# Kernel tuning notes

Hardware: AMD Instinct MI355X
Metric: run time of the kernel (lower is better)

## Reference

```python
import math
import jax, jax.numpy as jnp
import numpy as np

HIDDEN = 1024
N_HEADS = 16
HEAD_DIM = HIDDEN // N_HEADS
SEQ = 2048
BATCH = 2
MAX_SEQ = 2048
N_LAYERS = 4
ALPHA = 0.3
TOPK_FACTOR = 2
GAMMA = 0.5
M_FREQ = math.ceil(MAX_SEQ / 2) + 1  # rfft length


def _sample_indices(layer_idx):
    # FrequencyRampSampler.get_sample_indices (layer_idx is a static python int)
    l = layer_idx + 1
    M, L = M_FREQ, N_LAYERS
    if ALPHA > 1.0 / L:
        p = int(M * (1 - ALPHA) * (1 - (l - 1) / (L - 1))) if L > 1 else 0
        q = int(p + ALPHA * M)
    else:
        p = int(M * (1 - l / L))
        q = int(p + M / L)
    p = max(0, min(p, M - 1))
    q = max(p + 1, min(q, M))
    return p, q


def setup_inputs() -> dict:
    key = jax.random.key(0)
    ks = jax.random.split(key, 10)
    hidden_states = jax.random.normal(ks[0], (BATCH, SEQ, HIDDEN), jnp.float32)
    # causal additive mask [B,1,N,N]
    causal = jnp.tril(jnp.ones((SEQ, SEQ), jnp.float32))
    attention_mask = jnp.where(causal > 0, 0.0, -1e9).astype(jnp.float32)
    attention_mask = jnp.broadcast_to(attention_mask[None, None], (BATCH, 1, SEQ, SEQ))
    s = 0.02
    Wq = jax.random.normal(ks[1], (HIDDEN, HIDDEN), jnp.float32) * s
    Wk = jax.random.normal(ks[2], (HIDDEN, HIDDEN), jnp.float32) * s
    Wv = jax.random.normal(ks[3], (HIDDEN, HIDDEN), jnp.float32) * s
    Wo = jax.random.normal(ks[4], (HIDDEN, HIDDEN), jnp.float32) * s
    bq = jnp.zeros((HIDDEN,), jnp.float32)
    bk = jnp.zeros((HIDDEN,), jnp.float32)
    bv = jnp.zeros((HIDDEN,), jnp.float32)
    bo = jnp.zeros((HIDDEN,), jnp.float32)
    return dict(hidden_states=hidden_states, attention_mask=attention_mask,
                Wq=Wq, bq=bq, Wk=Wk, bk=bk, Wv=Wv, bv=bv, Wo=Wo, bo=bo,
                layer_idx=1)


def _forward(hidden_states, attention_mask, Wq, bq, Wk, bk, Wv, bv, Wo, bo, layer_idx):
    B, N, D = hidden_states.shape
    p, q = _sample_indices(layer_idx)
    Q = hidden_states @ Wq.T + bq
    K = hidden_states @ Wk.T + bk
    V = hidden_states @ Wv.T + bv

    # ---- time-domain branch: FFT -> band-select -> IFFT -> SDPA ----
    def band_filter(X):
        Xf = jnp.fft.rfft(X, axis=1)  # [B, M, D] complex64
        Xp = jnp.zeros_like(Xf).at[:, p:q, :].set(Xf[:, p:q, :])
        return jnp.fft.irfft(Xp, n=N, axis=1)

    Qt = band_filter(Q).reshape(B, N, N_HEADS, HEAD_DIM).transpose(0, 2, 1, 3)
    Kt = band_filter(K).reshape(B, N, N_HEADS, HEAD_DIM).transpose(0, 2, 1, 3)
    Vt = band_filter(V).reshape(B, N, N_HEADS, HEAD_DIM).transpose(0, 2, 1, 3)
    scores = jnp.einsum('bhnd,bhmd->bhnm', Qt, Kt) / math.sqrt(HEAD_DIM)
    scores = scores + attention_mask
    probs = jax.nn.softmax(scores, axis=-1)
    time_out = jnp.einsum('bhnm,bhmd->bhnd', probs, Vt)
    time_out = time_out.transpose(0, 2, 1, 3).reshape(B, N, D)

    # ---- frequency-domain branch: autocorrelation + top-k delay aggregation ----
    Qf = jnp.fft.rfft(Q, axis=1)
    Kf = jnp.fft.rfft(K, axis=1)
    corr = jnp.zeros_like(Qf).at[:, p:q, :].set(Qf[:, p:q, :] * jnp.conj(Kf[:, p:q, :]))
    R = jnp.fft.irfft(corr, n=N, axis=1)          # [B, N, D]
    R_mean = R.mean(axis=-1)                       # [B, N]
    k = min(max(1, int(TOPK_FACTOR * math.log(N + 1))), N)
    top_R, top_idx = jax.lax.top_k(R_mean, k)      # [B, k]
    attn_w = jax.nn.softmax(top_R, axis=-1)        # [B, k]
    # rolled index: (n - tau) mod N, for each of the k delays
    idx = (jnp.arange(N)[None, None, :] - top_idx[:, :, None]) % N   # [B, k, N]
    gathered = jnp.take_along_axis(V[:, None, :, :], idx[..., None], axis=2)  # [B, k, N, D]
    freq_out = jnp.einsum('bk,bknd->bnd', attn_w, gathered)

    out = GAMMA * time_out + (1.0 - GAMMA) * freq_out
    return out @ Wo.T + bo


def reference(hidden_states, attention_mask, Wq, bq, Wk, bk, Wv, bv, Wo, bo, layer_idx):
    return _forward(hidden_states, attention_mask, Wq, bq, Wk, bk, Wv, bv, Wo, bo, layer_idx)
```

## Files before the change

kernel.cpp:

```cpp
#include <hip/hip_runtime.h>
#include <hip/hip_bf16.h>

#define BATCHN 2
#define SEQ    2048
#define HID    1024
#define NHEADS 16
#define HD     64
#define P_LO   478
#define NF     307
#define NF2    614
#define NFP    640
#define KTOP   15
#define DPI    3.14159265358979323846

typedef __bf16 bf16_t;
typedef bf16_t v8bf __attribute__((ext_vector_type(8)));
typedef bf16_t v4bf __attribute__((ext_vector_type(4)));
typedef float  v4f  __attribute__((ext_vector_type(4)));

#define MFMA(a,b,c) __builtin_amdgcn_mfma_f32_16x16x32_bf16(a,b,c,0,0,0)

#define GLDS(gp, lp) __builtin_amdgcn_global_load_lds( \
    (const __attribute__((address_space(1))) void*)(gp), \
    (__attribute__((address_space(3))) void*)(lp), 16, 0, 0)

__launch_bounds__(256)
__global__ void detect_kernel(const unsigned short* __restrict__ x0,
                              const unsigned short* __restrict__ x1,
                              int* __restrict__ flag) {
    int t = threadIdx.x, bad = 0;
    for (int i = t; i < 8192; i += 256) {
        unsigned e0 = (x0[i] >> 7) & 0xFF; if (e0 >= 0x90) bad++;
        unsigned e1 = (x1[i] >> 7) & 0xFF; if (e1 >= 0x90) bad++;
    }
    __shared__ int s[256];
    s[t] = bad; __syncthreads();
    for (int st = 128; st; st >>= 1) { if (t < st) s[t] += s[t + st]; __syncthreads(); }
    if (t == 0) *flag = (s[0] > 64) ? 1 : 0;
}

__launch_bounds__(256)
__global__ void tab_kernel(bf16_t* __restrict__ Ahi, bf16_t* __restrict__ Alo,
                           bf16_t* __restrict__ Gt) {
    __shared__ float T[64 * 65];
    int t = threadIdx.x;
    int m0 = blockIdx.x * 64, r0 = blockIdx.y * 64;
    int m = t >> 2, rb = (t & 3) * 16;
    {
        v8bf g0, g1;
        #pragma unroll
        for (int i = 0; i < 16; i++) {
            int r = r0 + rb + i;
            float v = 0.f;
            if (r < NF2) {
                int f  = P_LO + (r < NF ? r : r - NF);
                int ph = (f * (m0 + m)) & (SEQ - 1);
                float ang = (float)(2.0 * DPI / SEQ) * (float)ph;
                float sn, cs;
                sincosf(ang, &sn, &cs);
                v = (r < NF) ? cs : sn;
            }
            T[(rb + i) * 65 + m] = v;
            bf16_t gv = (bf16_t)(v * (float)(2.0 / SEQ));
            if (i < 8) g0[i] = gv; else g1[i - 8] = gv;
        }
        *(v8bf*)&Gt[(size_t)(m0 + m) * NFP + r0 + rb]     = g0;
        *(v8bf*)&Gt[(size_t)(m0 + m) * NFP + r0 + rb + 8] = g1;
    }
    __syncthreads();
    int r = t >> 2, mb = (t & 3) * 16;
    v8bf h0, h1, l0, l1;
    #pragma unroll
    for (int i = 0; i < 16; i++) {
        float v = T[r * 65 + mb + i];
        bf16_t hh = (bf16_t)v;
        bf16_t ll = (bf16_t)(v - (float)hh);
        if (i < 8) { h0[i] = hh; l0[i] = ll; } else { h1[i - 8] = hh; l1[i - 8] = ll; }
    }
    size_t ro = (size_t)(r0 + r) * SEQ + m0 + mb;
    *(v8bf*)&Ahi[ro]     = h0;  *(v8bf*)&Ahi[ro + 8] = h1;
    *(v8bf*)&Alo[ro]     = l0;  *(v8bf*)&Alo[ro + 8] = l1;
}

__launch_bounds__(256)
__global__ void norm_x_kernel(const int* __restrict__ flag, const void* __restrict__ Xv,
                              bf16_t* __restrict__ Xh, bf16_t* __restrict__ XTh,
                              bf16_t* __restrict__ XTl) {
    int fl = *flag;
    __shared__ float T[64 * 65];
    int t = threadIdx.x;
    int R0 = blockIdx.y * 64, C0 = blockIdx.x * 64;
    int r = t >> 2;
    #pragma unroll
    for (int it = 0; it < 2; it++) {
        int c = (t & 3) * 8 + it * 32;
        float x[8];
        if (fl) {
            const float* p = (const float*)Xv + (size_t)(R0 + r) * HID + C0 + c;
            #pragma unroll
            for (int e = 0; e < 8; e++) x[e] = p[e];
        } else {
            const bf16_t* p = (const bf16_t*)Xv + (size_t)(R0 + r) * HID + C0 + c;
            #pragma unroll
            for (int e = 0; e < 8; e++) x[e] = (float)p[e];
        }
        v8bf h;
        #pragma unroll
        for (int e = 0; e < 8; e++) { h[e] = (bf16_t)x[e]; T[(r) * 65 + c + e] = x[e]; }
        *(v8bf*)&Xh[(size_t)(R0 + r) * HID + C0 + c] = h;
    }
    __syncthreads();
    int b  = blockIdx.y >> 5;
    int Rl = R0 - b * SEQ;
    int d  = t >> 2;
    #pragma unroll
    for (int it = 0; it < 2; it++) {
        int n = (t & 3) * 8 + it * 32;
        v8bf h, l;
        #pragma unroll
        for (int e = 0; e < 8; e++) {
            float x = T[(n + e) * 65 + d];
            bf16_t hh = (bf16_t)x;
            h[e] = hh; l[e] = (bf16_t)(x - (float)hh);
        }
        size_t off = ((size_t)b * HID + C0 + d) * SEQ + Rl + n;
        *(v8bf*)&XTh[off] = h;
        *(v8bf*)&XTl[off] = l;
    }
}

__launch_bounds__(256)
__global__ void gemm128_nt(const int* __restrict__ flag, const bf16_t* __restrict__ A,
                           const void* __restrict__ Braw, const void* __restrict__ biasraw,
                           void* __restrict__ Out, int outmode) {
    int fl = *flag;
    __shared__ __align__(16) bf16_t As[128 * 32];
    __shared__ __align__(16) bf16_t Bs[128 * 32];
    int t = threadIdx.x, wave = t >> 6, lane = t & 63;
    int lrow = lane & 15, quad = lane >> 4;
    int m0 = blockIdx.y * 128, n0 = blockIdx.x * 128;
    int wm = (wave >> 1) * 64, wn = (wave & 1) * 64;
    int grow = lane >> 2, gcol = (lane & 3) * 8;
    v4f acc[4][4] = {};
    for (int k0 = 0; k0 < HID; k0 += 32) {
        __syncthreads();
        GLDS(&A[(size_t)(m0 + wave * 32 + grow) * HID + k0 + gcol],      &As[(wave * 32) * 32]);
        GLDS(&A[(size_t)(m0 + wave * 32 + 16 + grow) * HID + k0 + gcol], &As[(wave * 32 + 16) * 32]);
        if (!fl) {
            const bf16_t* B = (const bf16_t*)Braw;
            GLDS(&B[(size_t)(n0 + wave * 32 + grow) * HID + k0 + gcol],      &Bs[(wave * 32) * 32]);
            GLDS(&B[(size_t)(n0 + wave * 32 + 16 + grow) * HID + k0 + gcol], &Bs[(wave * 32 + 16) * 32]);
        } else {
            const float* B = (const float*)Braw;
            #pragma unroll
            for (int i2 = 0; i2 < 2; i2++) {
                int row = (t >> 2) + 64 * i2, col = (t & 3) * 8;
                const float* p = &B[(size_t)(n0 + row) * HID + k0 + col];
                v8bf h;
                #pragma unroll
                for (int e = 0; e < 8; e++) h[e] = (bf16_t)p[e];
                *(v8bf*)&Bs[row * 32 + col] = h;
            }
        }
        __syncthreads();
        v8bf a[4], b[4];
        #pragma unroll
        for (int i = 0; i < 4; i++) a[i] = *(v8bf*)&As[(wm + i * 16 + lrow) * 32 + quad * 8];
        #pragma unroll
        for (int j = 0; j < 4; j++) b[j] = *(v8bf*)&Bs[(wn + j * 16 + lrow) * 32 + quad * 8];
        #pragma unroll
        for (int i = 0; i < 4; i++)
        #pragma unroll
        for (int j = 0; j < 4; j++) acc[i][j] = MFMA(a[i], b[j], acc[i][j]);
    }
    #pragma unroll
    for (int i = 0; i < 4; i++)
    #pragma unroll
    for (int j = 0; j < 4; j++) {
        int col = n0 + wn + 16 * j + lrow;
        float bvv = fl ? ((const float*)biasraw)[col] : (float)((const bf16_t*)biasraw)[col];
        #pragma unroll
        for (int rg = 0; rg < 4; rg++) {
            int row = m0 + wm + 16 * i + quad * 4 + rg;
            float v = acc[i][j][rg] + bvv;
            size_t off = (size_t)row * HID + col;
            if (outmode == 1 && fl) ((float*)Out)[off] = v;
            else ((bf16_t*)Out)[off] = (bf16_t)v;
        }
    }
}

__launch_bounds__(256)
__global__ void band_fwd(const bf16_t* __restrict__ Ahi, const bf16_t* __restrict__ Alo,
                         const bf16_t* __restrict__ XTh, const bf16_t* __restrict__ XTl,
                         bf16_t* __restrict__ Xfh, bf16_t* __restrict__ Xfl) {
    __shared__ __align__(16) bf16_t Ah[64 * 32], Al[64 * 32], Bh[64 * 32], Bl[64 * 32];
    int t = threadIdx.x, wave = t >> 6, lane = t & 63;
    int lrow = lane & 15, quad = lane >> 4;
    int m0 = blockIdx.y * 64, n0 = blockIdx.x * 64, b = blockIdx.z;
    int wm = (wave >> 1) * 32, wn = (wave & 1) * 32;
    int srow = t >> 2, scol = (t & 3) * 8;
    const bf16_t* bth = XTh + (size_t)b * HID * SEQ;
    const bf16_t* btl = XTl + (size_t)b * HID * SEQ;
    v4f acc[2][2] = {};
    for (int k0 = 0; k0 < SEQ; k0 += 32) {
        __syncthreads();
        GLDS(&Ahi[(size_t)(m0 + srow) * SEQ + k0 + scol], &Ah[srow * 32 + scol]);
        GLDS(&Alo[(size_t)(m0 + srow) * SEQ + k0 + scol], &Al[srow * 32 + scol]);
        GLDS(&bth[(size_t)(n0 + srow) * SEQ + k0 + scol], &Bh[srow * 32 + scol]);
        GLDS(&btl[(size_t)(n0 + srow) * SEQ + k0 + scol], &Bl[srow * 32 + scol]);
        __syncthreads();
        v8bf ah0 = *(v8bf*)&Ah[(wm + lrow) * 32 + quad * 8];
        v8bf ah1 = *(v8bf*)&Ah[(wm + 16 + lrow) * 32 + quad * 8];
        v8bf al0 = *(v8bf*)&Al[(wm + lrow) * 32 + quad * 8];
        v8bf al1 = *(v8bf*)&Al[(wm + 16 + lrow) * 32 + quad * 8];
        v8bf bh0 = *(v8bf*)&Bh[(wn + lrow) * 32 + quad * 8];
        v8bf bh1 = *(v8bf*)&Bh[(wn + 16 + lrow) * 32 + quad * 8];
        v8bf bl0 = *(v8bf*)&Bl[(wn + lrow) * 32 + quad * 8];
        v8bf bl1 = *(v8bf*)&Bl[(wn + 16 + lrow) * 32 + quad * 8];
        acc[0][0] = MFMA(ah0, bh0, acc[0][0]); acc[0][0] = MFMA(ah0, bl0, acc[0][0]); acc[0][0] = MFMA(al0, bh0, acc[0][0]);
        acc[0][1] = MFMA(ah0, bh1, acc[0][1]); acc[0][1] = MFMA(ah0, bl1, acc[0][1]); acc[0][1] = MFMA(al0, bh1, acc[0][1]);
        acc[1][0] = MFMA(ah1, bh0, acc[1][0]); acc[1][0] = MFMA(ah1, bl0, acc[1][0]); acc[1][0] = MFMA(al1, bh0, acc[1][0]);
        acc[1][1] = MFMA(ah1, bh1, acc[1][1]); acc[1][1] = MFMA(ah1, bl1, acc[1][1]); acc[1][1] = MFMA(al1, bh1, acc[1][1]);
    }
    bf16_t* oh = Xfh + (size_t)b * NFP * HID;
    bf16_t* ol = Xfl + (size_t)b * NFP * HID;
    #pragma unroll
    for (int i = 0; i < 2; i++)
    #pragma unroll
    for (int j = 0; j < 2; j++) {
        int col = n0 + wn + 16 * j + lrow;
        #pragma unroll
        for (int rg = 0; rg < 4; rg++) {
            int row = m0 + wm + 16 * i + quad * 4 + rg;
            float v = acc[i][j][rg];
            bf16_t h = (bf16_t)v;
            oh[(size_t)row * HID + col] = h;
            ol[(size_t)row * HID + col] = (bf16_t)(v - (float)h);
        }
    }
}

__launch_bounds__(256)
__global__ void proj_f(const int* __restrict__ flag, const bf16_t* __restrict__ Xfh,
                       const bf16_t* __restrict__ Xfl,
                       const void* __restrict__ Wq_, const void* __restrict__ Wk_,
                       const void* __restrict__ Wv_,
                       bf16_t* __restrict__ Qfh, bf16_t* __restrict__ Qfl,
                       bf16_t* __restrict__ Kfh, bf16_t* __restrict__ Kfl,
                       bf16_t* __restrict__ QfT, bf16_t* __restrict__ KfT,
                       bf16_t* __restrict__ VfT) {
    int fl = *flag;
    int bz = blockIdx.z, b = bz & 1, sel = bz >> 1;
    const void* Wraw = sel == 0 ? Wq_ : sel == 1 ? Wk_ : Wv_;
    bf16_t* Ch = sel == 0 ? Qfh : Kfh;
    bf16_t* Cl = sel == 0 ? Qfl : Kfl;
    bf16_t* CT = sel == 0 ? QfT : sel == 1 ? KfT : VfT;
    bool qk = sel < 2;
    __shared__ __align__(16) bf16_t Ah[64 * 32], Al[64 * 32], Bh[64 * 32], Bl[64 * 32];
    int t = threadIdx.x, wave = t >> 6, lane = t & 63;
    int lrow = lane & 15, quad = lane >> 4;
    int m0 = blockIdx.y * 64, n0 = blockIdx.x * 64;
    int wm = (wave >> 1) * 32, wn = (wave & 1) * 32;
    int srow = t >> 2, scol = (t & 3) * 8;
    const size_t zo = (size_t)b * NFP * HID;
    v4f acc[2][2] = {};
    for (int k0 = 0; k0 < HID; k0 += 32) {
        __syncthreads();
        GLDS(&Xfh[zo + (size_t)(m0 + srow) * HID + k0 + scol], &Ah[srow * 32 + scol]);
        GLDS(&Xfl[zo + (size_t)(m0 + srow) * HID + k0 + scol], &Al[srow * 32 + scol]);
        {
            float xb[8];
            if (fl) {
                const float* p = (const float*)Wraw + (size_t)(n0 + srow) * HID + k0 + scol;
                #pragma unroll
                for (int e = 0; e < 8; e++) xb[e] = p[e];
            } else {
                const bf16_t* p = (const bf16_t*)Wraw + (size_t)(n0 + srow) * HID + k0 + scol;
                #pragma unroll
                for (int e = 0; e < 8; e++) xb[e] = (float)p[e];
            }
            v8bf h, l;
            #pragma unroll
            for (int e = 0; e < 8; e++) {
                bf16_t hh = (bf16_t)xb[e];
                h[e] = hh; l[e] = (bf16_t)(xb[e] - (float)hh);
            }
            *(v8bf*)&Bh[srow * 32 + scol] = h;
            *(v8bf*)&Bl[srow * 32 + scol] = l;
        }
        __syncthreads();
        v8bf ah0 = *(v8bf*)&Ah[(wm + lrow) * 32 + quad * 8];
        v8bf ah1 = *(v8bf*)&Ah[(wm + 16 + lrow) * 32 + quad * 8];
        v8bf al0 = *(v8bf*)&Al[(wm + lrow) * 32 + quad * 8];
        v8bf al1 = *(v8bf*)&Al[(wm + 16 + lrow) * 32 + quad * 8];
        v8bf bh0 = *(v8bf*)&Bh[(wn + lrow) * 32 + quad * 8];
        v8bf bh1 = *(v8bf*)&Bh[(wn + 16 + lrow) * 32 + quad * 8];
        acc[0][0] = MFMA(ah0, bh0, acc[0][0]); acc[0][0] = MFMA(al0, bh0, acc[0][0]);
        acc[0][1] = MFMA(ah0, bh1, acc[0][1]); acc[0][1] = MFMA(al0, bh1, acc[0][1]);
        acc[1][0] = MFMA(ah1, bh0, acc[1][0]); acc[1][0] = MFMA(al1, bh0, acc[1][0]);
        acc[1][1] = MFMA(ah1, bh1, acc[1][1]); acc[1][1] = MFMA(al1, bh1, acc[1][1]);
        if (qk) {
            v8bf bl0 = *(v8bf*)&Bl[(wn + lrow) * 32 + quad * 8];
            v8bf bl1 = *(v8bf*)&Bl[(wn + 16 + lrow) * 32 + quad * 8];
            acc[0][0] = MFMA(ah0, bl0, acc[0][0]);
            acc[0][1] = MFMA(ah0, bl1, acc[0][1]);
            acc[1][0] = MFMA(ah1, bl0, acc[1][0]);
            acc[1][1] = MFMA(ah1, bl1, acc[1][1]);
        }
    }
    #pragma unroll
    for (int i = 0; i < 2; i++)
    #pragma unroll
    for (int j = 0; j < 2; j++) {
        int col = n0 + wn + 16 * j + lrow;
        v4bf pk;
        #pragma unroll
        for (int rg = 0; rg < 4; rg++) {
            int row = m0 + wm + 16 * i + quad * 4 + rg;
            float v = acc[i][j][rg];
            bf16_t h = (bf16_t)v;
            pk[rg] = h;
            if (qk) {
                Ch[zo + (size_t)row * HID + col] = h;
                Cl[zo + (size_t)row * HID + col] = (bf16_t)(v - (float)h);
            }
        }
        *(v4bf*)&CT[zo + (size_t)col * NFP + m0 + wm + 16 * i + quad * 4] = pk;
    }
}

__launch_bounds__(256)
__global__ void inv128_f(const bf16_t* __restrict__ Gt, const bf16_t* __restrict__ QfT,
                         const bf16_t* __restrict__ KfT, const bf16_t* __restrict__ VfT,
                         bf16_t* __restrict__ Qt, bf16_t* __restrict__ Kt,
                         bf16_t* __restrict__ VTd) {
    int bz = blockIdx.z, b = bz & 1, sel = bz >> 1;
    const bf16_t* BT = (sel == 0 ? QfT : sel == 1 ? KfT : VfT) + (size_t)b * HID * NFP;
    bf16_t* Out = sel == 0 ? Qt : sel == 1 ? Kt : VTd;
    bool trans = (sel == 2);
    __shared__ __align__(16) bf16_t As[128 * 32];
    __shared__ __align__(16) bf16_t Bs[128 * 32];
    int t = threadIdx.x, wave = t >> 6, lane = t & 63;
    int lrow = lane & 15, quad = lane >> 4;
    int m0 = blockIdx.y * 128, n0 = blockIdx.x * 128;
    int wm = (wave >> 1) * 64, wn = (wave & 1) * 64;
    int grow = lane >> 2, gcol = (lane & 3) * 8;
    v4f acc[4][4] = {};
    for (int k0 = 0; k0 < NFP; k0 += 32) {
        __syncthreads();
        GLDS(&Gt[(size_t)(m0 + wave * 32 + grow) * NFP + k0 + gcol],      &As[(wave * 32) * 32]);
        GLDS(&Gt[(size_t)(m0 + wave * 32 + 16 + grow) * NFP + k0 + gcol], &As[(wave * 32 + 16) * 32]);
        GLDS(&BT[(size_t)(n0 + wave * 32 + grow) * NFP + k0 + gcol],      &Bs[(wave * 32) * 32]);
        GLDS(&BT[(size_t)(n0 + wave * 32 + 16 + grow) * NFP + k0 + gcol], &Bs[(wave * 32 + 16) * 32]);
        __syncthreads();
        v8bf a[4], bfr[4];
        #pragma unroll
        for (int i = 0; i < 4; i++) a[i]   = *(v8bf*)&As[(wm + i * 16 + lrow) * 32 + quad * 8];
        #pragma unroll
        for (int j = 0; j < 4; j++) bfr[j] = *(v8bf*)&Bs[(wn + j * 16 + lrow) * 32 + quad * 8];
        #pragma unroll
        for (int i = 0; i < 4; i++)
        #pragma unroll
        for (int j = 0; j < 4; j++) acc[i][j] = MFMA(a[i], bfr[j], acc[i][j]);
    }
    #pragma unroll
    for (int i = 0; i < 4; i++)
    #pragma unroll
    for (int j = 0; j < 4; j++) {
        int col = n0 + wn + 16 * j + lrow;
        if (trans) {
            v4bf pk;
            #pragma unroll
            for (int rg = 0; rg < 4; rg++) pk[rg] = (bf16_t)acc[i][j][rg];
            *(v4bf*)&Out[((size_t)b * HID + col) * SEQ + m0 + wm + 16 * i + quad * 4] = pk;
        } else {
            #pragma unroll
            for (int rg = 0; rg < 4; rg++) {
                int row = m0 + wm + 16 * i + quad * 4 + rg;
                Out[(size_t)b * SEQ * HID + (size_t)row * HID + col] = (bf16_t)acc[i][j][rg];
            }
        }
    }
}

__launch_bounds__(256)
__global__ void attn_kernel(const bf16_t* __restrict__ Qt, const bf16_t* __restrict__ Kt,
                            const bf16_t* __restrict__ VT, bf16_t* __restrict__ TO) {
    __shared__ __align__(16) bf16_t Ks[2][64 * 72];
    __shared__ __align__(16) bf16_t Vs[2][64 * 72];
    __shared__ __align__(16) bf16_t Ps[4 * 16 * 72];
    int t = threadIdx.x, wave = t >> 6, lane = t & 63;
    int lrow = lane & 15, quad = lane >> 4;
    int h = blockIdx.y, b = blockIdx.z;
    int q0 = (gridDim.x - 1 - blockIdx.x) * 128;
    const size_t base = (size_t)b * SEQ * HID + (size_t)h * HD;
    const bf16_t* vb_ = VT + ((size_t)b * HID + h * HD) * SEQ;
    bf16_t* Pw = &Ps[wave * 16 * 72];

    v8bf qa[2][2];
    #pragma unroll
    for (int g = 0; g < 2; g++) {
        int qrow = q0 + g * 64 + wave * 16 + lrow;
        qa[g][0] = *(const v8bf*)&Qt[base + (size_t)qrow * HID + quad * 8];
        qa[g][1] = *(const v8bf*)&Qt[base + (size_t)qrow * HID + 32 + quad * 8];
    }
    v4f o[2][4] = {};
    float m_i[2] = {-1e30f, -1e30f}, l_i[2] = {0.f, 0.f};
    int srow = t >> 2, cc0 = (t & 3) * 16;
    int nch = q0 / 64 + 2;
    v8bf kp0 = *(const v8bf*)&Kt[base + (size_t)srow * HID + cc0];
    v8bf kp1 = *(const v8bf*)&Kt[base + (size_t)srow * HID + cc0 + 8];
    v8bf vp0 = *(const v8bf*)&vb_[(size_t)srow * SEQ + cc0];
    v8bf vp1 = *(const v8bf*)&vb_[(size_t)srow * SEQ + cc0 + 8];
    for (int c = 0; c < nch; c++) {
        int kb = c * 64;
        int cur = c & 1;
        *(v8bf*)&Ks[cur][srow * 72 + cc0]     = kp0;
        *(v8bf*)&Ks[cur][srow * 72 + cc0 + 8] = kp1;
        *(v8bf*)&Vs[cur][srow * 72 + cc0]     = vp0;
        *(v8bf*)&Vs[cur][srow * 72 + cc0 + 8] = vp1;
        __syncthreads();
        if (c + 1 < nch) {
            int kb2 = kb + 64;
            kp0 = *(const v8bf*)&Kt[base + (size_t)(kb2 + srow) * HID + cc0];
            kp1 = *(const v8bf*)&Kt[base + (size_t)(kb2 + srow) * HID + cc0 + 8];
            vp0 = *(const v8bf*)&vb_[(size_t)srow * SEQ + kb2 + cc0];
            vp1 = *(const v8bf*)&vb_[(size_t)srow * SEQ + kb2 + cc0 + 8];
        }
        v8bf kA[4][2], vB[4][2];
        #pragma unroll
        for (int ct = 0; ct < 4; ct++) {
            kA[ct][0] = *(v8bf*)&Ks[cur][(ct * 16 + lrow) * 72 + quad * 8];
            kA[ct][1] = *(v8bf*)&Ks[cur][(ct * 16 + lrow) * 72 + 32 + quad * 8];
            vB[ct][0] = *(v8bf*)&Vs[cur][(ct * 16 + lrow) * 72 + quad * 8];
            vB[ct][1] = *(v8bf*)&Vs[cur][(ct * 16 + lrow) * 72 + 32 + quad * 8];
        }
        #pragma unroll
        for (int g = 0; g < 2; g++) {
            if (kb >= q0 + g * 64 + 64) continue;
            bool masked = (kb == q0 + g * 64);
            v4f s[4];
            #pragma unroll
            for (int ct = 0; ct < 4; ct++) {
                v4f z = {};
                z = MFMA(kA[ct][0], qa[g][0], z);
                s[ct] = MFMA(kA[ct][1], qa[g][1], z);
            }
            float sv[4][4];
            float mx = -1e30f;
            #pragma unroll
            for (int ct = 0; ct < 4; ct++)
            #pragma unroll
            for (int r = 0; r < 4; r++) {
                float x = s[ct][r] * 0.125f;
                if (masked && (ct * 16 + quad * 4 + r > wave * 16 + lrow)) x = -1e30f;
                sv[ct][r] = x;
                mx = fmaxf(mx, x);
            }
            mx = fmaxf(mx, __shfl_xor(mx, 16));
            mx = fmaxf(mx, __shfl_xor(mx, 32));
            float mnew = fmaxf(m_i[g], mx);
            float alpha = __expf(m_i[g] - mnew);
            m_i[g] = mnew;
            float rs = 0.f;
            #pragma unroll
            for (int ct = 0; ct < 4; ct++)
            #pragma unroll
            for (int r = 0; r < 4; r++) { float p = __expf(sv[ct][r] - mnew); sv[ct][r] = p; rs += p; }
            rs += __shfl_xor(rs, 16);
            rs += __shfl_xor(rs, 32);
            l_i[g] = l_i[g] * alpha + rs;
            #pragma unroll
            for (int r = 0; r < 4; r++) {
                float ar = __shfl(alpha, quad * 4 + r);
                #pragma unroll
                for (int dt = 0; dt < 4; dt++) o[g][dt][r] *= ar;
            }
            #pragma unroll
            for (int ct = 0; ct < 4; ct++) {
                v4bf pk;
                #pragma unroll
                for (int r = 0; r < 4; r++) pk[r] = (bf16_t)sv[ct][r];
                *(v4bf*)&Pw[lrow * 72 + ct * 16 + quad * 4] = pk;
            }
            v8bf pa0 = *(v8bf*)&Pw[lrow * 72 + quad * 8];
            v8bf pa1 = *(v8bf*)&Pw[lrow * 72 + 32 + quad * 8];
            #pragma unroll
            for (int dt = 0; dt < 4; dt++) {
                o[g][dt] = MFMA(pa0, vB[dt][0], o[g][dt]);
                o[g][dt] = MFMA(pa1, vB[dt][1], o[g][dt]);
            }
        }
        __syncthreads();
    }
    #pragma unroll
    for (int g = 0; g < 2; g++)
    #pragma unroll
    for (int r = 0; r < 4; r++) {
        float lr = __shfl(l_i[g], quad * 4 + r);
        int qg = q0 + g * 64 + wave * 16 + quad * 4 + r;
        #pragma unroll
        for (int dt = 0; dt < 4; dt++)
            TO[base + (size_t)qg * HID + dt * 16 + lrow] = (bf16_t)(o[g][dt][r] / lr);
    }
}

__launch_bounds__(256)
__global__ void sfreq_kernel(const bf16_t* __restrict__ Qh, const bf16_t* __restrict__ Ql,
                             const bf16_t* __restrict__ Kh, const bf16_t* __restrict__ Kl,
                             float* __restrict__ Sre, float* __restrict__ Sim) {
    int f = blockIdx.x, b = blockIdx.y, t = threadIdx.x;
    const size_t oc = ((size_t)b * NFP + f) * HID;
    const size_t os = ((size_t)b * NFP + NF + f) * HID;
    float re = 0.f, im = 0.f;
    for (int d = t; d < HID; d += 256) {
        float cq = (float)Qh[oc + d] + (float)Ql[oc + d];
        float sq = (float)Qh[os + d] + (float)Ql[os + d];
        float ck = (float)Kh[oc + d] + (float)Kl[oc + d];
        float sk = (float)Kh[os + d] + (float)Kl[os + d];
        re += cq * ck + sq * sk;
        im += cq * sk - sq * ck;
    }
    #pragma unroll
    for (int msk = 1; msk < 64; msk <<= 1) { re += __shfl_xor(re, msk); im += __shfl_xor(im, msk); }
    __shared__ float rbuf[8];
    int wave = t >> 6, lane = t & 63;
    if (lane == 0) { rbuf[wave] = re; rbuf[4 + wave] = im; }
    __syncthreads();
    if (t == 0) {
        Sre[b * NF + f] = rbuf[0] + rbuf[1] + rbuf[2] + rbuf[3];
        Sim[b * NF + f] = rbuf[4] + rbuf[5] + rbuf[6] + rbuf[7];
    }
}

__launch_bounds__(256)
__global__ void rmean_kernel(const float* __restrict__ Sre, const float* __restrict__ Sim,
                             float* __restrict__ Rm) {
    int b = blockIdx.y;
    int nl = threadIdx.x & 63, part = threadIdx.x >> 6;
    int n = blockIdx.x * 64 + nl;
    __shared__ float sr[NF], si[NF];
    __shared__ float red[4][64];
    for (int i = threadIdx.x; i < NF; i += 256) { sr[i] = Sre[b * NF + i]; si[i] = Sim[b * NF + i]; }
    __syncthreads();
    float acc = 0.f;
    for (int r = part; r < NF; r += 4) {
        int ph = ((P_LO + r) * n) & (SEQ - 1);
        float ang = (float)(2.0 * DPI / SEQ) * (float)ph;
        float sn, cs;
        sincosf(ang, &sn, &cs);
        acc += sr[r] * cs - si[r] * sn;
    }
    red[part][nl] = acc;
    __syncthreads();
    if (part == 0) {
        float s = red[0][nl] + red[1][nl] + red[2][nl] + red[3][nl];
        Rm[b * SEQ + n] = s * (float)(2.0 / ((double)SEQ * (double)HID));
    }
}

__launch_bounds__(64)
__global__ void topk_kernel(const float* __restrict__ Rm, int* __restrict__ Ti,
                            float* __restrict__ Tw) {
    int b = blockIdx.x, lane = threadIdx.x;
    float v[32];
    #pragma unroll
    for (int j = 0; j < 32; j++) v[j] = Rm[b * SEQ + j * 64 + lane];
    float selv[KTOP];
    int   seli[KTOP];
    for (int kk = 0; kk < KTOP; kk++) {
        float best = -INFINITY; int bi = lane;
        #pragma unroll
        for (int j = 0; j < 32; j++) {
            float x = v[j];
            if (x > best) { best = x; bi = j * 64 + lane; }
        }
        #pragma unroll
        for (int off = 1; off < 64; off <<= 1) {
            float ov = __shfl_xor(best, off);
            int   oi = __shfl_xor(bi, off);
            if (ov > best || (ov == best && oi < bi)) { best = ov; bi = oi; }
        }
        selv[kk] = best; seli[kk] = bi;
        if (lane == (bi & 63)) v[bi >> 6] = -INFINITY;
    }
    float mx = selv[0];
    #pragma unroll
    for (int i = 1; i < KTOP; i++) mx = fmaxf(mx, selv[i]);
    float s = 0.f, e[KTOP];
    #pragma unroll
    for (int i = 0; i < KTOP; i++) { e[i] = __expf(selv[i] - mx); s += e[i]; }
    if (lane < KTOP) { Tw[b * KTOP + lane] = e[lane] / s; Ti[b * KTOP + lane] = seli[lane]; }
}

__launch_bounds__(256)
__global__ void combine_kernel(const bf16_t* __restrict__ TO, const bf16_t* __restrict__ V,
                               const int* __restrict__ Ti, const float* __restrict__ Tw,
                               bf16_t* __restrict__ Yc) {
    int b = blockIdx.z, n = blockIdx.y;
    int d = blockIdx.x * 256 + threadIdx.x;
    __shared__ int   ti[KTOP];
    __shared__ float tw[KTOP];
    if (threadIdx.x < KTOP) { ti[threadIdx.x] = Ti[b * KTOP + threadIdx.x]; tw[threadIdx.x] = Tw[b * KTOP + threadIdx.x]; }
    __syncthreads();
    float fo = 0.f;
    #pragma unroll
    for (int kk = 0; kk < KTOP; kk++) {
        int nn = (n - ti[kk] + SEQ) & (SEQ - 1);
        fo += tw[kk] * (float)V[((size_t)b * SEQ + nn) * HID + d];
    }
    size_t off = ((size_t)b * SEQ + n) * HID + d;
    Yc[off] = (bf16_t)(0.5f * (float)TO[off] + 0.5f * fo);
}

extern "C" void kernel_launch(void* const* d_in, const int* in_sizes, int n_in,
                              void* d_out, int out_size, void* d_ws, size_t ws_size,
                              hipStream_t stream) {
    (void)in_sizes; (void)n_in; (void)out_size; (void)ws_size;
    const void* X  = d_in[0];
    const void* Wq = d_in[2];
    const void* Wk = d_in[4];
    const void* Wv = d_in[6];
    const void* bv = d_in[7];
    const void* Wo = d_in[8];
    const void* bo = d_in[9];

    const size_t SZ_X   = (size_t)BATCHN * SEQ * HID * 2;
    const size_t SZ_TAB = (size_t)NFP * SEQ * 2;
    const size_t SZ_F   = (size_t)BATCHN * NFP * HID * 2;
    char* w = (char*)d_ws;
    bf16_t* Xh  = (bf16_t*)(w);
    bf16_t* Xfh = (bf16_t*)(w);
    bf16_t* Xfl = (bf16_t*)(w + SZ_F);
    bf16_t* Qt  = (bf16_t*)(w);
    bf16_t* Yc  = (bf16_t*)(w);
    bf16_t* XTh = (bf16_t*)(w + SZ_X);
    bf16_t* Qfh = (bf16_t*)(w + SZ_X);
    bf16_t* Qfl = (bf16_t*)(w + SZ_X + SZ_F);
    bf16_t* Kfh = (bf16_t*)(w + SZ_X + 2 * SZ_F);
    bf16_t* Kt  = (bf16_t*)(w + SZ_X);
    bf16_t* XTl = (bf16_t*)(w + 2 * SZ_X);
    bf16_t* Kfl = (bf16_t*)(w + 2 * SZ_X);
    bf16_t* QfT = (bf16_t*)(w + 2 * SZ_X + SZ_F);
    bf16_t* KfT = (bf16_t*)(w + 2 * SZ_X + 2 * SZ_F);
    bf16_t* TO  = (bf16_t*)(w + 2 * SZ_X);
    bf16_t* Vm  = (bf16_t*)(w + 3 * SZ_X);
    bf16_t* Gt  = (bf16_t*)(w + 4 * SZ_X);
    bf16_t* Ahi = (bf16_t*)(w + 4 * SZ_X + SZ_TAB);
    bf16_t* Alo = (bf16_t*)(w + 4 * SZ_X + 2 * SZ_TAB);
    bf16_t* VfT = (bf16_t*)(w + 4 * SZ_X + SZ_TAB);
    char*  sm  = w + 4 * SZ_X + 3 * SZ_TAB;
    int*   flag = (int*)sm;
    float* Sre  = (float*)(sm + 256);
    float* Sim  = (float*)(sm + 256 + 4096);
    float* Rm   = (float*)(sm + 256 + 8192);
    int*   Ti   = (int*)  (sm + 256 + 8192 + 16384);
    float* Tw   = (float*)(sm + 256 + 8192 + 16384 + 256);
    bf16_t* VT  = (bf16_t*)d_out;

    detect_kernel<<<1, 256, 0, stream>>>((const unsigned short*)X, (const unsigned short*)Wq, flag);
    tab_kernel<<<dim3(SEQ / 64, NFP / 64), 256, 0, stream>>>(Ahi, Alo, Gt);
    norm_x_kernel<<<dim3(16, 64), 256, 0, stream>>>(flag, X, Xh, XTh, XTl);
    gemm128_nt<<<dim3(8, 32), 256, 0, stream>>>(flag, Xh, Wv, bv, Vm, 0);
    band_fwd<<<dim3(16, NFP / 64, BATCHN), 256, 0, stream>>>(Ahi, Alo, XTh, XTl, Xfh, Xfl);
    proj_f<<<dim3(16, NFP / 64, 6), 256, 0, stream>>>(flag, Xfh, Xfl, Wq, Wk, Wv,
                                                      Qfh, Qfl, Kfh, Kfl, QfT, KfT, VfT);
    sfreq_kernel<<<dim3(NF, BATCHN), 256, 0, stream>>>(Qfh, Qfl, Kfh, Kfl, Sre, Sim);
    rmean_kernel<<<dim3(SEQ / 64, BATCHN), 256, 0, stream>>>(Sre, Sim, Rm);
    topk_kernel<<<BATCHN, 64, 0, stream>>>(Rm, Ti, Tw);
    inv128_f<<<dim3(8, 16, 6), 256, 0, stream>>>(Gt, QfT, KfT, VfT, Qt, Kt, VT);
    attn_kernel<<<dim3(SEQ / 128, NHEADS, BATCHN), 256, 0, stream>>>(Qt, Kt, VT, TO);
    combine_kernel<<<dim3(HID / 256, SEQ, BATCHN), 256, 0, stream>>>(TO, Vm, Ti, Tw, Yc);
    gemm128_nt<<<dim3(8, 32), 256, 0, stream>>>(flag, Yc, Wo, bo, d_out, 1);
}
```

Measured before the change: 433.7 us.

## Merge independent stages into block-indexed mega kernels and vectorize combine

Folds detect, table generation, input normalization and the V projection into one launch whose blocks dispatch on block index, with each block re-deriving the input-dtype flag locally. The inverse transform is merged with the rmean reduction, and top-k with attention, in two more such kernels. The V GEMM now reads and converts X directly, dropping the Xh staging copy. The combine kernel handles 8 elements per thread with vector loads, and attention uses exp2f. The goal is fewer launches and better overlap of independent work, at the cost of redundant flag detection in many blocks and mixed block shapes sharing one launch.

```diff
diff --git a/kernel.cpp b/kernel.cpp
--- a/kernel.cpp
+++ b/kernel.cpp
@@ -12,6 +12,7 @@
 #define NFP    640
 #define KTOP   15
 #define DPI    3.14159265358979323846
+#define L2E    1.44269504f
 
 typedef __bf16 bf16_t;
 typedef bf16_t v8bf __attribute__((ext_vector_type(8)));
@@ -24,27 +25,25 @@
     (const __attribute__((address_space(1))) void*)(gp), \
     (__attribute__((address_space(3))) void*)(lp), 16, 0, 0)
 
-__launch_bounds__(256)
-__global__ void detect_kernel(const unsigned short* __restrict__ x0,
-                              const unsigned short* __restrict__ x1,
-                              int* __restrict__ flag) {
+__device__ __forceinline__ int self_detect(const unsigned short* __restrict__ x, char* SM) {
+    int* s = (int*)SM;
     int t = threadIdx.x, bad = 0;
     for (int i = t; i < 8192; i += 256) {
-        unsigned e0 = (x0[i] >> 7) & 0xFF; if (e0 >= 0x90) bad++;
-        unsigned e1 = (x1[i] >> 7) & 0xFF; if (e1 >= 0x90) bad++;
-    }
-    __shared__ int s[256];
+        unsigned e = (x[i] >> 7) & 0xFF;
+        if (e >= 0x90) bad++;
+    }
     s[t] = bad; __syncthreads();
     for (int st = 128; st; st >>= 1) { if (t < st) s[t] += s[t + st]; __syncthreads(); }
-    if (t == 0) *flag = (s[0] > 64) ? 1 : 0;
-}
-
-__launch_bounds__(256)
-__global__ void tab_kernel(bf16_t* __restrict__ Ahi, bf16_t* __restrict__ Alo,
-                           bf16_t* __restrict__ Gt) {
-    __shared__ float T[64 * 65];
+    int r = (s[0] > 32) ? 1 : 0;
+    __syncthreads();
+    return r;
+}
+
+__device__ __forceinline__ void tab_body(int bi, char* SM, bf16_t* Ahi, bf16_t* Alo,
+                                         bf16_t* Gt) {
+    float* T = (float*)SM;
     int t = threadIdx.x;
-    int m0 = blockIdx.x * 64, r0 = blockIdx.y * 64;
+    int m0 = (bi & 31) * 64, r0 = (bi >> 5) * 64;
     int m = t >> 2, rb = (t & 3) * 16;
     {
         v8bf g0, g1;
@@ -82,14 +81,11 @@
     *(v8bf*)&Alo[ro]     = l0;  *(v8bf*)&Alo[ro + 8] = l1;
 }
 
-__launch_bounds__(256)
-__global__ void norm_x_kernel(const int* __restrict__ flag, const void* __restrict__ Xv,
-                              bf16_t* __restrict__ Xh, bf16_t* __restrict__ XTh,
-                              bf16_t* __restrict__ XTl) {
-    int fl = *flag;
-    __shared__ float T[64 * 65];
+__device__ __forceinline__ void norm_body(int bi, int fl, char* SM, const void* Xv,
+                                          bf16_t* XTh, bf16_t* XTl) {
+    float* T = (float*)SM;
     int t = threadIdx.x;
-    int R0 = blockIdx.y * 64, C0 = blockIdx.x * 64;
+    int C0 = (bi & 15) * 64, R0 = (bi >> 4) * 64;
     int r = t >> 2;
     #pragma unroll
     for (int it = 0; it < 2; it++) {
@@ -104,13 +100,11 @@
             #pragma unroll
             for (int e = 0; e < 8; e++) x[e] = (float)p[e];
         }
-        v8bf h;
-        #pragma unroll
-        for (int e = 0; e < 8; e++) { h[e] = (bf16_t)x[e]; T[(r) * 65 + c + e] = x[e]; }
-        *(v8bf*)&Xh[(size_t)(R0 + r) * HID + C0 + c] = h;
+        #pragma unroll
+        for (int e = 0; e < 8; e++) T[r * 65 + c + e] = x[e];
     }
     __syncthreads();
-    int b  = blockIdx.y >> 5;
+    int b  = (R0 >= SEQ) ? 1 : 0;
     int Rl = R0 - b * SEQ;
     int d  = t >> 2;
     #pragma unroll
@@ -129,37 +123,39 @@
     }
 }
 
-__launch_bounds__(256)
-__global__ void gemm128_nt(const int* __restrict__ flag, const bf16_t* __restrict__ A,
-                           const void* __restrict__ Braw, const void* __restrict__ biasraw,
-                           void* __restrict__ Out, int outmode) {
-    int fl = *flag;
-    __shared__ __align__(16) bf16_t As[128 * 32];
-    __shared__ __align__(16) bf16_t Bs[128 * 32];
+__device__ __forceinline__ void gemmv_body(int bi, int fl, char* SM, const void* Xraw,
+                                           const void* Braw, const void* biasraw,
+                                           bf16_t* Out) {
+    bf16_t* As = (bf16_t*)SM;
+    bf16_t* Bs = (bf16_t*)(SM + 8192);
     int t = threadIdx.x, wave = t >> 6, lane = t & 63;
     int lrow = lane & 15, quad = lane >> 4;
-    int m0 = blockIdx.y * 128, n0 = blockIdx.x * 128;
+    int n0 = (bi & 7) * 128, m0 = (bi >> 3) * 128;
     int wm = (wave >> 1) * 64, wn = (wave & 1) * 64;
     int grow = lane >> 2, gcol = (lane & 3) * 8;
     v4f acc[4][4] = {};
     for (int k0 = 0; k0 < HID; k0 += 32) {
         __syncthreads();
-        GLDS(&A[(size_t)(m0 + wave * 32 + grow) * HID + k0 + gcol],      &As[(wave * 32) * 32]);
-        GLDS(&A[(size_t)(m0 + wave * 32 + 16 + grow) * HID + k0 + gcol], &As[(wave * 32 + 16) * 32]);
         if (!fl) {
+            const bf16_t* A = (const bf16_t*)Xraw;
             const bf16_t* B = (const bf16_t*)Braw;
+            GLDS(&A[(size_t)(m0 + wave * 32 + grow) * HID + k0 + gcol],      &As[(wave * 32) * 32]);
+            GLDS(&A[(size_t)(m0 + wave * 32 + 16 + grow) * HID + k0 + gcol], &As[(wave * 32 + 16) * 32]);
             GLDS(&B[(size_t)(n0 + wave * 32 + grow) * HID + k0 + gcol],      &Bs[(wave * 32) * 32]);
             GLDS(&B[(size_t)(n0 + wave * 32 + 16 + grow) * HID + k0 + gcol], &Bs[(wave * 32 + 16) * 32]);
         } else {
+            const float* A = (const float*)Xraw;
             const float* B = (const float*)Braw;
             #pragma unroll
             for (int i2 = 0; i2 < 2; i2++) {
                 int row = (t >> 2) + 64 * i2, col = (t & 3) * 8;
-                const float* p = &B[(size_t)(n0 + row) * HID + k0 + col];
-                v8bf h;
+                const float* pa = &A[(size_t)(m0 + row) * HID + k0 + col];
+                const float* pb = &B[(size_t)(n0 + row) * HID + k0 + col];
+                v8bf ha, hb;
                 #pragma unroll
-                for (int e = 0; e < 8; e++) h[e] = (bf16_t)p[e];
-                *(v8bf*)&Bs[row * 32 + col] = h;
+                for (int e = 0; e < 8; e++) { ha[e] = (bf16_t)pa[e]; hb[e] = (bf16_t)pb[e]; }
+                *(v8bf*)&As[row * 32 + col] = ha;
+                *(v8bf*)&Bs[row * 32 + col] = hb;
             }
         }
         __syncthreads();
@@ -182,11 +178,41 @@
         #pragma unroll
         for (int rg = 0; rg < 4; rg++) {
             int row = m0 + wm + 16 * i + quad * 4 + rg;
-            float v = acc[i][j][rg] + bvv;
-            size_t off = (size_t)row * HID + col;
-            if (outmode == 1 && fl) ((float*)Out)[off] = v;
-            else ((bf16_t*)Out)[off] = (bf16_t)v;
-        }
+            Out[(size_t)row * HID + col] = (bf16_t)(acc[i][j][rg] + bvv);
+        }
+    }
+}
+
+__launch_bounds__(256)
+__global__ void mega1_kernel(const void* __restrict__ X, const void* __restrict__ Wq,
+                             const void* __restrict__ Wv, const void* __restrict__ bv,
+                             bf16_t* __restrict__ Vm,
+                             bf16_t* __restrict__ Ahi, bf16_t* __restrict__ Alo,
+                             bf16_t* __restrict__ Gt,
+                             bf16_t* __restrict__ XTh, bf16_t* __restrict__ XTl,
+                             int* __restrict__ flag) {
+    __shared__ __align__(16) char SM[17408];
+    int bx = blockIdx.x;
+    if (bx < 256) {
+        int fl = self_detect((const unsigned short*)X, SM);
+        gemmv_body(bx, fl, SM, X, Wv, bv, Vm);
+    } else if (bx < 576) {
+        tab_body(bx - 256, SM, Ahi, Alo, Gt);
+    } else if (bx < 1600) {
+        int fl = self_detect((const unsigned short*)X, SM);
+        norm_body(bx - 576, fl, SM, X, XTh, XTl);
+    } else {
+        const unsigned short* x0 = (const unsigned short*)X;
+        const unsigned short* x1 = (const unsigned short*)Wq;
+        int* s = (int*)SM;
+        int t = threadIdx.x, bad = 0;
+        for (int i = t; i < 8192; i += 256) {
+            unsigned e0 = (x0[i] >> 7) & 0xFF; if (e0 >= 0x90) bad++;
+            unsigned e1 = (x1[i] >> 7) & 0xFF; if (e1 >= 0x90) bad++;
+        }
+        s[t] = bad; __syncthreads();
+        for (int st = 128; st; st >>= 1) { if (t < st) s[t] += s[t + st]; __syncthreads(); }
+        if (t == 0) *flag = (s[0] > 64) ? 1 : 0;
     }
 }
 
@@ -331,182 +357,6 @@
 }
 
 __launch_bounds__(256)
-__global__ void inv128_f(const bf16_t* __restrict__ Gt, const bf16_t* __restrict__ QfT,
-                         const bf16_t* __restrict__ KfT, const bf16_t* __restrict__ VfT,
-                         bf16_t* __restrict__ Qt, bf16_t* __restrict__ Kt,
-                         bf16_t* __restrict__ VTd) {
-    int bz = blockIdx.z, b = bz & 1, sel = bz >> 1;
-    const bf16_t* BT = (sel == 0 ? QfT : sel == 1 ? KfT : VfT) + (size_t)b * HID * NFP;
-    bf16_t* Out = sel == 0 ? Qt : sel == 1 ? Kt : VTd;
-    bool trans = (sel == 2);
-    __shared__ __align__(16) bf16_t As[128 * 32];
-    __shared__ __align__(16) bf16_t Bs[128 * 32];
-    int t = threadIdx.x, wave = t >> 6, lane = t & 63;
-    int lrow = lane & 15, quad = lane >> 4;
-    int m0 = blockIdx.y * 128, n0 = blockIdx.x * 128;
-    int wm = (wave >> 1) * 64, wn = (wave & 1) * 64;
-    int grow = lane >> 2, gcol = (lane & 3) * 8;
-    v4f acc[4][4] = {};
-    for (int k0 = 0; k0 < NFP; k0 += 32) {
-        __syncthreads();
-        GLDS(&Gt[(size_t)(m0 + wave * 32 + grow) * NFP + k0 + gcol],      &As[(wave * 32) * 32]);
-        GLDS(&Gt[(size_t)(m0 + wave * 32 + 16 + grow) * NFP + k0 + gcol], &As[(wave * 32 + 16) * 32]);
-        GLDS(&BT[(size_t)(n0 + wave * 32 + grow) * NFP + k0 + gcol],      &Bs[(wave * 32) * 32]);
-        GLDS(&BT[(size_t)(n0 + wave * 32 + 16 + grow) * NFP + k0 + gcol], &Bs[(wave * 32 + 16) * 32]);
-        __syncthreads();
-        v8bf a[4], bfr[4];
-        #pragma unroll
-        for (int i = 0; i < 4; i++) a[i]   = *(v8bf*)&As[(wm + i * 16 + lrow) * 32 + quad * 8];
-        #pragma unroll
-        for (int j = 0; j < 4; j++) bfr[j] = *(v8bf*)&Bs[(wn + j * 16 + lrow) * 32 + quad * 8];
-        #pragma unroll
-        for (int i = 0; i < 4; i++)
-        #pragma unroll
-        for (int j = 0; j < 4; j++) acc[i][j] = MFMA(a[i], bfr[j], acc[i][j]);
-    }
-    #pragma unroll
-    for (int i = 0; i < 4; i++)
-    #pragma unroll
-    for (int j = 0; j < 4; j++) {
-        int col = n0 + wn + 16 * j + lrow;
-        if (trans) {
-            v4bf pk;
-            #pragma unroll
-            for (int rg = 0; rg < 4; rg++) pk[rg] = (bf16_t)acc[i][j][rg];
-            *(v4bf*)&Out[((size_t)b * HID + col) * SEQ + m0 + wm + 16 * i + quad * 4] = pk;
-        } else {
-            #pragma unroll
-            for (int rg = 0; rg < 4; rg++) {
-                int row = m0 + wm + 16 * i + quad * 4 + rg;
-                Out[(size_t)b * SEQ * HID + (size_t)row * HID + col] = (bf16_t)acc[i][j][rg];
-            }
-        }
-    }
-}
-
-__launch_bounds__(256)
-__global__ void attn_kernel(const bf16_t* __restrict__ Qt, const bf16_t* __restrict__ Kt,
-                            const bf16_t* __restrict__ VT, bf16_t* __restrict__ TO) {
-    __shared__ __align__(16) bf16_t Ks[2][64 * 72];
-    __shared__ __align__(16) bf16_t Vs[2][64 * 72];
-    __shared__ __align__(16) bf16_t Ps[4 * 16 * 72];
-    int t = threadIdx.x, wave = t >> 6, lane = t & 63;
-    int lrow = lane & 15, quad = lane >> 4;
-    int h = blockIdx.y, b = blockIdx.z;
-    int q0 = (gridDim.x - 1 - blockIdx.x) * 128;
-    const size_t base = (size_t)b * SEQ * HID + (size_t)h * HD;
-    const bf16_t* vb_ = VT + ((size_t)b * HID + h * HD) * SEQ;
-    bf16_t* Pw = &Ps[wave * 16 * 72];
-
-    v8bf qa[2][2];
-    #pragma unroll
-    for (int g = 0; g < 2; g++) {
-        int qrow = q0 + g * 64 + wave * 16 + lrow;
-        qa[g][0] = *(const v8bf*)&Qt[base + (size_t)qrow * HID + quad * 8];
-        qa[g][1] = *(const v8bf*)&Qt[base + (size_t)qrow * HID + 32 + quad * 8];
-    }
-    v4f o[2][4] = {};
-    float m_i[2] = {-1e30f, -1e30f}, l_i[2] = {0.f, 0.f};
-    int srow = t >> 2, cc0 = (t & 3) * 16;
-    int nch = q0 / 64 + 2;
-    v8bf kp0 = *(const v8bf*)&Kt[base + (size_t)srow * HID + cc0];
-    v8bf kp1 = *(const v8bf*)&Kt[base + (size_t)srow * HID + cc0 + 8];
-    v8bf vp0 = *(const v8bf*)&vb_[(size_t)srow * SEQ + cc0];
-    v8bf vp1 = *(const v8bf*)&vb_[(size_t)srow * SEQ + cc0 + 8];
-    for (int c = 0; c < nch; c++) {
-        int kb = c * 64;
-        int cur = c & 1;
-        *(v8bf*)&Ks[cur][srow * 72 + cc0]     = kp0;
-        *(v8bf*)&Ks[cur][srow * 72 + cc0 + 8] = kp1;
-        *(v8bf*)&Vs[cur][srow * 72 + cc0]     = vp0;
-        *(v8bf*)&Vs[cur][srow * 72 + cc0 + 8] = vp1;
-        __syncthreads();
-        if (c + 1 < nch) {
-            int kb2 = kb + 64;
-            kp0 = *(const v8bf*)&Kt[base + (size_t)(kb2 + srow) * HID + cc0];
-            kp1 = *(const v8bf*)&Kt[base + (size_t)(kb2 + srow) * HID + cc0 + 8];
-            vp0 = *(const v8bf*)&vb_[(size_t)srow * SEQ + kb2 + cc0];
-            vp1 = *(const v8bf*)&vb_[(size_t)srow * SEQ + kb2 + cc0 + 8];
-        }
-        v8bf kA[4][2], vB[4][2];
-        #pragma unroll
-        for (int ct = 0; ct < 4; ct++) {
-            kA[ct][0] = *(v8bf*)&Ks[cur][(ct * 16 + lrow) * 72 + quad * 8];
-            kA[ct][1] = *(v8bf*)&Ks[cur][(ct * 16 + lrow) * 72 + 32 + quad * 8];
-            vB[ct][0] = *(v8bf*)&Vs[cur][(ct * 16 + lrow) * 72 + quad * 8];
-            vB[ct][1] = *(v8bf*)&Vs[cur][(ct * 16 + lrow) * 72 + 32 + quad * 8];
-        }
-        #pragma unroll
-        for (int g = 0; g < 2; g++) {
-            if (kb >= q0 + g * 64 + 64) continue;
-            bool masked = (kb == q0 + g * 64);
-            v4f s[4];
-            #pragma unroll
-            for (int ct = 0; ct < 4; ct++) {
-                v4f z = {};
-                z = MFMA(kA[ct][0], qa[g][0], z);
-                s[ct] = MFMA(kA[ct][1], qa[g][1], z);
-            }
-            float sv[4][4];
-            float mx = -1e30f;
-            #pragma unroll
-            for (int ct = 0; ct < 4; ct++)
-            #pragma unroll
-            for (int r = 0; r < 4; r++) {
-                float x = s[ct][r] * 0.125f;
-                if (masked && (ct * 16 + quad * 4 + r > wave * 16 + lrow)) x = -1e30f;
-                sv[ct][r] = x;
-                mx = fmaxf(mx, x);
-            }
-            mx = fmaxf(mx, __shfl_xor(mx, 16));
-            mx = fmaxf(mx, __shfl_xor(mx, 32));
-            float mnew = fmaxf(m_i[g], mx);
-            float alpha = __expf(m_i[g] - mnew);
-            m_i[g] = mnew;
-            float rs = 0.f;
-            #pragma unroll
-            for (int ct = 0; ct < 4; ct++)
-            #pragma unroll
-            for (int r = 0; r < 4; r++) { float p = __expf(sv[ct][r] - mnew); sv[ct][r] = p; rs += p; }
-            rs += __shfl_xor(rs, 16);
-            rs += __shfl_xor(rs, 32);
-            l_i[g] = l_i[g] * alpha + rs;
-            #pragma unroll
-            for (int r = 0; r < 4; r++) {
-                float ar = __shfl(alpha, quad * 4 + r);
-                #pragma unroll
-                for (int dt = 0; dt < 4; dt++) o[g][dt][r] *= ar;
-            }
-            #pragma unroll
-            for (int ct = 0; ct < 4; ct++) {
-                v4bf pk;
-                #pragma unroll
-                for (int r = 0; r < 4; r++) pk[r] = (bf16_t)sv[ct][r];
-                *(v4bf*)&Pw[lrow * 72 + ct * 16 + quad * 4] = pk;
-            }
-            v8bf pa0 = *(v8bf*)&Pw[lrow * 72 + quad * 8];
-            v8bf pa1 = *(v8bf*)&Pw[lrow * 72 + 32 + quad * 8];
-            #pragma unroll
-            for (int dt = 0; dt < 4; dt++) {
-                o[g][dt] = MFMA(pa0, vB[dt][0], o[g][dt]);
-                o[g][dt] = MFMA(pa1, vB[dt][1], o[g][dt]);
-            }
-        }
-        __syncthreads();
-    }
-    #pragma unroll
-    for (int g = 0; g < 2; g++)
-    #pragma unroll
-    for (int r = 0; r < 4; r++) {
-        float lr = __shfl(l_i[g], quad * 4 + r);
-        int qg = q0 + g * 64 + wave * 16 + quad * 4 + r;
-        #pragma unroll
-        for (int dt = 0; dt < 4; dt++)
-            TO[base + (size_t)qg * HID + dt * 16 + lrow] = (bf16_t)(o[g][dt][r] / lr);
-    }
-}
-
-__launch_bounds__(256)
 __global__ void sfreq_kernel(const bf16_t* __restrict__ Qh, const bf16_t* __restrict__ Ql,
                              const bf16_t* __restrict__ Kh, const bf16_t* __restrict__ Kl,
                              float* __restrict__ Sre, float* __restrict__ Sim) {
@@ -534,14 +384,67 @@
     }
 }
 
-__launch_bounds__(256)
-__global__ void rmean_kernel(const float* __restrict__ Sre, const float* __restrict__ Sim,
-                             float* __restrict__ Rm) {
-    int b = blockIdx.y;
+__device__ __forceinline__ void inv_body(int bi, char* SM, const bf16_t* Gt,
+                                         const bf16_t* QfT, const bf16_t* KfT,
+                                         const bf16_t* VfT, bf16_t* Qt, bf16_t* Kt,
+                                         bf16_t* VTd) {
+    int b = (bi >> 7) & 1, sel = bi >> 8;
+    const bf16_t* BT = (sel == 0 ? QfT : sel == 1 ? KfT : VfT) + (size_t)b * HID * NFP;
+    bf16_t* Out = sel == 0 ? Qt : sel == 1 ? Kt : VTd;
+    bool trans = (sel == 2);
+    bf16_t* As = (bf16_t*)SM;
+    bf16_t* Bs = (bf16_t*)(SM + 8192);
+    int t = threadIdx.x, wave = t >> 6, lane = t & 63;
+    int lrow = lane & 15, quad = lane >> 4;
+    int n0 = (bi & 7) * 128, m0 = ((bi >> 3) & 15) * 128;
+    int wm = (wave >> 1) * 64, wn = (wave & 1) * 64;
+    int grow = lane >> 2, gcol = (lane & 3) * 8;
+    v4f acc[4][4] = {};
+    for (int k0 = 0; k0 < NFP; k0 += 32) {
+        __syncthreads();
+        GLDS(&Gt[(size_t)(m0 + wave * 32 + grow) * NFP + k0 + gcol],      &As[(wave * 32) * 32]);
+        GLDS(&Gt[(size_t)(m0 + wave * 32 + 16 + grow) * NFP + k0 + gcol], &As[(wave * 32 + 16) * 32]);
+        GLDS(&BT[(size_t)(n0 + wave * 32 + grow) * NFP + k0 + gcol],      &Bs[(wave * 32) * 32]);
+        GLDS(&BT[(size_t)(n0 + wave * 32 + 16 + grow) * NFP + k0 + gcol], &Bs[(wave * 32 + 16) * 32]);
+        __syncthreads();
+        v8bf a[4], bfr[4];
+        #pragma unroll
+        for (int i = 0; i < 4; i++) a[i]   = *(v8bf*)&As[(wm + i * 16 + lrow) * 32 + quad * 8];
+        #pragma unroll
+        for (int j = 0; j < 4; j++) bfr[j] = *(v8bf*)&Bs[(wn + j * 16 + lrow) * 32 + quad * 8];
+        #pragma unroll
+        for (int i = 0; i < 4; i++)
+        #pragma unroll
+        for (int j = 0; j < 4; j++) acc[i][j] = MFMA(a[i], bfr[j], acc[i][j]);
+    }
+    #pragma unroll
+    for (int i = 0; i < 4; i++)
+    #pragma unroll
+    for (int j = 0; j < 4; j++) {
+        int col = n0 + wn + 16 * j + lrow;
+        if (trans) {
+            v4bf pk;
+            #pragma unroll
+            for (int rg = 0; rg < 4; rg++) pk[rg] = (bf16_t)acc[i][j][rg];
+            *(v4bf*)&Out[((size_t)b * HID + col) * SEQ + m0 + wm + 16 * i + quad * 4] = pk;
+        } else {
+            #pragma unroll
+            for (int rg = 0; rg < 4; rg++) {
+                int row = m0 + wm + 16 * i + quad * 4 + rg;
+                Out[(size_t)b * SEQ * HID + (size_t)row * HID + col] = (bf16_t)acc[i][j][rg];
+            }
+        }
+    }
+}
+
+__device__ __forceinline__ void rmean_body(int bi, char* SM, const float* Sre,
+                                           const float* Sim, float* Rm) {
+    int b = bi >> 5;
+    float* sr  = (float*)SM;
+    float* si  = sr + NF;
+    float* red = si + NF;
     int nl = threadIdx.x & 63, part = threadIdx.x >> 6;
-    int n = blockIdx.x * 64 + nl;
-    __shared__ float sr[NF], si[NF];
-    __shared__ float red[4][64];
+    int n = (bi & 31) * 64 + nl;
     for (int i = threadIdx.x; i < NF; i += 256) { sr[i] = Sre[b * NF + i]; si[i] = Sim[b * NF + i]; }
     __syncthreads();
     float acc = 0.f;
@@ -552,18 +455,153 @@
         sincosf(ang, &sn, &cs);
         acc += sr[r] * cs - si[r] * sn;
     }
-    red[part][nl] = acc;
+    red[part * 64 + nl] = acc;
     __syncthreads();
     if (part == 0) {
-        float s = red[0][nl] + red[1][nl] + red[2][nl] + red[3][nl];
+        float s = red[nl] + red[64 + nl] + red[128 + nl] + red[192 + nl];
         Rm[b * SEQ + n] = s * (float)(2.0 / ((double)SEQ * (double)HID));
     }
 }
 
-__launch_bounds__(64)
-__global__ void topk_kernel(const float* __restrict__ Rm, int* __restrict__ Ti,
-                            float* __restrict__ Tw) {
-    int b = blockIdx.x, lane = threadIdx.x;
+__launch_bounds__(256)
+__global__ void mega5_kernel(const bf16_t* __restrict__ Gt, const bf16_t* __restrict__ QfT,
+                             const bf16_t* __restrict__ KfT, const bf16_t* __restrict__ VfT,
+                             bf16_t* __restrict__ Qt, bf16_t* __restrict__ Kt,
+                             bf16_t* __restrict__ VTd,
+                             const float* __restrict__ Sre, const float* __restrict__ Sim,
+                             float* __restrict__ Rm) {
+    __shared__ __align__(16) char SM[16384];
+    int bx = blockIdx.x;
+    if (bx < 768) inv_body(bx, SM, Gt, QfT, KfT, VfT, Qt, Kt, VTd);
+    else          rmean_body(bx - 768, SM, Sre, Sim, Rm);
+}
+
+__device__ __forceinline__ void attn_body(int bi, char* SM, const bf16_t* Qt,
+                                          const bf16_t* Kt, const bf16_t* VT, bf16_t* TO) {
+    bf16_t* Ks = (bf16_t*)SM;
+    bf16_t* Vs = (bf16_t*)(SM + 18432);
+    bf16_t* Ps = (bf16_t*)(SM + 36864);
+    int t = threadIdx.x, wave = t >> 6, lane = t & 63;
+    int lrow = lane & 15, quad = lane >> 4;
+    int h = (bi >> 4) & 15, b = bi >> 8;
+    int q0 = (15 - (bi & 15)) * 128;
+    const size_t base = (size_t)b * SEQ * HID + (size_t)h * HD;
+    const bf16_t* vb_ = VT + ((size_t)b * HID + h * HD) * SEQ;
+    bf16_t* Pw = &Ps[wave * 16 * 72];
+
+    v8bf qa[2][2];
+    #pragma unroll
+    for (int g = 0; g < 2; g++) {
+        int qrow = q0 + g * 64 + wave * 16 + lrow;
+        qa[g][0] = *(const v8bf*)&Qt[base + (size_t)qrow * HID + quad * 8];
+        qa[g][1] = *(const v8bf*)&Qt[base + (size_t)qrow * HID + 32 + quad * 8];
+    }
+    v4f o[2][4] = {};
+    float m_i[2] = {-1e30f, -1e30f}, l_i[2] = {0.f, 0.f};
+    int srow = t >> 2, cc0 = (t & 3) * 16;
+    int nch = q0 / 64 + 2;
+    v8bf kp0 = *(const v8bf*)&Kt[base + (size_t)srow * HID + cc0];
+    v8bf kp1 = *(const v8bf*)&Kt[base + (size_t)srow * HID + cc0 + 8];
+    v8bf vp0 = *(const v8bf*)&vb_[(size_t)srow * SEQ + cc0];
+    v8bf vp1 = *(const v8bf*)&vb_[(size_t)srow * SEQ + cc0 + 8];
+    const float SC = 0.125f * L2E;
+    for (int c = 0; c < nch; c++) {
+        int kb = c * 64;
+        int cur = c & 1;
+        bf16_t* Kc = &Ks[cur * 64 * 72];
+        bf16_t* Vc = &Vs[cur * 64 * 72];
+        *(v8bf*)&Kc[srow * 72 + cc0]     = kp0;
+        *(v8bf*)&Kc[srow * 72 + cc0 + 8] = kp1;
+        *(v8bf*)&Vc[srow * 72 + cc0]     = vp0;
+        *(v8bf*)&Vc[srow * 72 + cc0 + 8] = vp1;
+        __syncthreads();
+        if (c + 1 < nch) {
+            int kb2 = kb + 64;
+            kp0 = *(const v8bf*)&Kt[base + (size_t)(kb2 + srow) * HID + cc0];
+            kp1 = *(const v8bf*)&Kt[base + (size_t)(kb2 + srow) * HID + cc0 + 8];
+            vp0 = *(const v8bf*)&vb_[(size_t)srow * SEQ + kb2 + cc0];
+            vp1 = *(const v8bf*)&vb_[(size_t)srow * SEQ + kb2 + cc0 + 8];
+        }
+        v8bf kA[4][2], vB[4][2];
+        #pragma unroll
+        for (int ct = 0; ct < 4; ct++) {
+            kA[ct][0] = *(v8bf*)&Kc[(ct * 16 + lrow) * 72 + quad * 8];
+            kA[ct][1] = *(v8bf*)&Kc[(ct * 16 + lrow) * 72 + 32 + quad * 8];
+            vB[ct][0] = *(v8bf*)&Vc[(ct * 16 + lrow) * 72 + quad * 8];
+            vB[ct][1] = *(v8bf*)&Vc[(ct * 16 + lrow) * 72 + 32 + quad * 8];
+        }
+        #pragma unroll
+        for (int g = 0; g < 2; g++) {
+            if (kb >= q0 + g * 64 + 64) continue;
+            bool masked = (kb == q0 + g * 64);
+            v4f s[4];
+            #pragma unroll
+            for (int ct = 0; ct < 4; ct++) {
+                v4f z = {};
+                z = MFMA(kA[ct][0], qa[g][0], z);
+                s[ct] = MFMA(kA[ct][1], qa[g][1], z);
+            }
+            float sv[4][4];
+            float mx = -1e30f;
+            #pragma unroll
+            for (int ct = 0; ct < 4; ct++)
+            #pragma unroll
+            for (int r = 0; r < 4; r++) {
+                float x = s[ct][r] * SC;
+                if (masked && (ct * 16 + quad * 4 + r > wave * 16 + lrow)) x = -1e30f;
+                sv[ct][r] = x;
+                mx = fmaxf(mx, x);
+            }
+            mx = fmaxf(mx, __shfl_xor(mx, 16));
+            mx = fmaxf(mx, __shfl_xor(mx, 32));
+            float mnew = fmaxf(m_i[g], mx);
+            float alpha = exp2f(m_i[g] - mnew);
+            m_i[g] = mnew;
+            float rs = 0.f;
+            #pragma unroll
+            for (int ct = 0; ct < 4; ct++)
+            #pragma unroll
+            for (int r = 0; r < 4; r++) { float p = exp2f(sv[ct][r] - mnew); sv[ct][r] = p; rs += p; }
+            rs += __shfl_xor(rs, 16);
+            rs += __shfl_xor(rs, 32);
+            l_i[g] = l_i[g] * alpha + rs;
+            #pragma unroll
+            for (int r = 0; r < 4; r++) {
+                float ar = __shfl(alpha, quad * 4 + r);
+                #pragma unroll
+                for (int dt = 0; dt < 4; dt++) o[g][dt][r] *= ar;
+            }
+            #pragma unroll
+            for (int ct = 0; ct < 4; ct++) {
+                v4bf pk;
+                #pragma unroll
+                for (int r = 0; r < 4; r++) pk[r] = (bf16_t)sv[ct][r];
+                *(v4bf*)&Pw[lrow * 72 + ct * 16 + quad * 4] = pk;
+            }
+            v8bf pa0 = *(v8bf*)&Pw[lrow * 72 + quad * 8];
+            v8bf pa1 = *(v8bf*)&Pw[lrow * 72 + 32 + quad * 8];
+            #pragma unroll
+            for (int dt = 0; dt < 4; dt++) {
+                o[g][dt] = MFMA(pa0, vB[dt][0], o[g][dt]);
+                o[g][dt] = MFMA(pa1, vB[dt][1], o[g][dt]);
+            }
+        }
+        __syncthreads();
+    }
+    #pragma unroll
+    for (int g = 0; g < 2; g++)
+    #pragma unroll
+    for (int r = 0; r < 4; r++) {
+        float lr = __shfl(l_i[g], quad * 4 + r);
+        int qg = q0 + g * 64 + wave * 16 + quad * 4 + r;
+        #pragma unroll
+        for (int dt = 0; dt < 4; dt++)
+            TO[base + (size_t)qg * HID + dt * 16 + lrow] = (bf16_t)(o[g][dt][r] / lr);
+    }
+}
+
+__device__ __forceinline__ void topk_body(int b, const float* Rm, int* Ti, float* Tw) {
+    int lane = threadIdx.x;
     float v[32];
     #pragma unroll
     for (int j = 0; j < 32; j++) v[j] = Rm[b * SEQ + j * 64 + lane];
@@ -595,23 +633,104 @@
 }
 
 __launch_bounds__(256)
+__global__ void mega6_kernel(const bf16_t* __restrict__ Qt, const bf16_t* __restrict__ Kt,
+                             const bf16_t* __restrict__ VT, bf16_t* __restrict__ TO,
+                             const float* __restrict__ Rm, int* __restrict__ Ti,
+                             float* __restrict__ Tw) {
+    __shared__ __align__(16) char SM[46080];
+    int bx = blockIdx.x;
+    if (bx < 512) attn_body(bx, SM, Qt, Kt, VT, TO);
+    else if (threadIdx.x < 64) topk_body(bx - 512, Rm, Ti, Tw);
+}
+
+__launch_bounds__(256)
 __global__ void combine_kernel(const bf16_t* __restrict__ TO, const bf16_t* __restrict__ V,
                                const int* __restrict__ Ti, const float* __restrict__ Tw,
                                bf16_t* __restrict__ Yc) {
-    int b = blockIdx.z, n = blockIdx.y;
-    int d = blockIdx.x * 256 + threadIdx.x;
+    int b = blockIdx.y;
     __shared__ int   ti[KTOP];
     __shared__ float tw[KTOP];
     if (threadIdx.x < KTOP) { ti[threadIdx.x] = Ti[b * KTOP + threadIdx.x]; tw[threadIdx.x] = Tw[b * KTOP + threadIdx.x]; }
     __syncthreads();
-    float fo = 0.f;
+    int idx = threadIdx.x * 8;
+    int r = idx >> 10, d = idx & 1023;
+    int n = blockIdx.x * 2 + r;
+    float fo[8] = {};
     #pragma unroll
     for (int kk = 0; kk < KTOP; kk++) {
         int nn = (n - ti[kk] + SEQ) & (SEQ - 1);
-        fo += tw[kk] * (float)V[((size_t)b * SEQ + nn) * HID + d];
+        v8bf vv = *(const v8bf*)&V[((size_t)b * SEQ + nn) * HID + d];
+        float w8 = tw[kk];
+        #pragma unroll
+        for (int e = 0; e < 8; e++) fo[e] += w8 * (float)vv[e];
     }
     size_t off = ((size_t)b * SEQ + n) * HID + d;
-    Yc[off] = (bf16_t)(0.5f * (float)TO[off] + 0.5f * fo);
+    v8bf to = *(const v8bf*)&TO[off];
+    v8bf y;
+    #pragma unroll
+    for (int e = 0; e < 8; e++) y[e] = (bf16_t)(0.5f * (float)to[e] + 0.5f * fo[e]);
+    *(v8bf*)&Yc[off] = y;
+}
+
+__launch_bounds__(256)
+__global__ void gemmO_kernel(const int* __restrict__ flag, const bf16_t* __restrict__ A,
+                             const void* __restrict__ Braw, const void* __restrict__ biasraw,
+                             void* __restrict__ Out) {
+    int fl = *flag;
+    __shared__ __align__(16) bf16_t As[128 * 32];
+    __shared__ __align__(16) bf16_t Bs[128 * 32];
+    int t = threadIdx.x, wave = t >> 6, lane = t & 63;
+    int lrow = lane & 15, quad = lane >> 4;
+    int m0 = blockIdx.y * 128, n0 = blockIdx.x * 128;
+    int wm = (wave >> 1) * 64, wn = (wave & 1) * 64;
+    int grow = lane >> 2, gcol = (lane & 3) * 8;
+    v4f acc[4][4] = {};
+    for (int k0 = 0; k0 < HID; k0 += 32) {
+        __syncthreads();
+        GLDS(&A[(size_t)(m0 + wave * 32 + grow) * HID + k0 + gcol],      &As[(wave * 32) * 32]);
+        GLDS(&A[(size_t)(m0 + wave * 32 + 16 + grow) * HID + k0 + gcol], &As[(wave * 32 + 16) * 32]);
+        if (!fl) {
+            const bf16_t* B = (const bf16_t*)Braw;
+            GLDS(&B[(size_t)(n0 + wave * 32 + grow) * HID + k0 + gcol],      &Bs[(wave * 32) * 32]);
+            GLDS(&B[(size_t)(n0 + wave * 32 + 16 + grow) * HID + k0 + gcol], &Bs[(wave * 32 + 16) * 32]);
+        } else {
+            const float* B = (const float*)Braw;
+            #pragma unroll
+            for (int i2 = 0; i2 < 2; i2++) {
+                int row = (t >> 2) + 64 * i2, col = (t & 3) * 8;
+                const float* p = &B[(size_t)(n0 + row) * HID + k0 + col];
+                v8bf h;
+                #pragma unroll
+                for (int e = 0; e < 8; e++) h[e] = (bf16_t)p[e];
+                *(v8bf*)&Bs[row * 32 + col] = h;
+            }
+        }
+        __syncthreads();
+        v8bf a[4], b[4];
+        #pragma unroll
+        for (int i = 0; i < 4; i++) a[i] = *(v8bf*)&As[(wm + i * 16 + lrow) * 32 + quad * 8];
+        #pragma unroll
+        for (int j = 0; j < 4; j++) b[j] = *(v8bf*)&Bs[(wn + j * 16 + lrow) * 32 + quad * 8];
+        #pragma unroll
+        for (int i = 0; i < 4; i++)
+        #pragma unroll
+        for (int j = 0; j < 4; j++) acc[i][j] = MFMA(a[i], b[j], acc[i][j]);
+    }
+    #pragma unroll
+    for (int i = 0; i < 4; i++)
+    #pragma unroll
+    for (int j = 0; j < 4; j++) {
+        int col = n0 + wn + 16 * j + lrow;
+        float bvv = fl ? ((const float*)biasraw)[col] : (float)((const bf16_t*)biasraw)[col];
+        #pragma unroll
+        for (int rg = 0; rg < 4; rg++) {
+            int row = m0 + wm + 16 * i + quad * 4 + rg;
+            float v = acc[i][j][rg] + bvv;
+            size_t off = (size_t)row * HID + col;
+            if (fl) ((float*)Out)[off] = v;
+            else ((bf16_t*)Out)[off] = (bf16_t)v;
+        }
+    }
 }
 
 extern "C" void kernel_launch(void* const* d_in, const int* in_sizes, int n_in,
@@ -630,7 +749,6 @@
     const size_t SZ_TAB = (size_t)NFP * SEQ * 2;
     const size_t SZ_F   = (size_t)BATCHN * NFP * HID * 2;
     char* w = (char*)d_ws;
-    bf16_t* Xh  = (bf16_t*)(w);
     bf16_t* Xfh = (bf16_t*)(w);
     bf16_t* Xfl = (bf16_t*)(w + SZ_F);
     bf16_t* Qt  = (bf16_t*)(w);
@@ -659,18 +777,13 @@
     float* Tw   = (float*)(sm + 256 + 8192 + 16384 + 256);
     bf16_t* VT  = (bf16_t*)d_out;
 
-    detect_kernel<<<1, 256, 0, stream>>>((const unsigned short*)X, (const unsigned short*)Wq, flag);
-    tab_kernel<<<dim3(SEQ / 64, NFP / 64), 256, 0, stream>>>(Ahi, Alo, Gt);
-    norm_x_kernel<<<dim3(16, 64), 256, 0, stream>>>(flag, X, Xh, XTh, XTl);
-    gemm128_nt<<<dim3(8, 32), 256, 0, stream>>>(flag, Xh, Wv, bv, Vm, 0);
+    mega1_kernel<<<1601, 256, 0, stream>>>(X, Wq, Wv, bv, Vm, Ahi, Alo, Gt, XTh, XTl, flag);
     band_fwd<<<dim3(16, NFP / 64, BATCHN), 256, 0, stream>>>(Ahi, Alo, XTh, XTl, Xfh, Xfl);
     proj_f<<<dim3(16, NFP / 64, 6), 256, 0, stream>>>(flag, Xfh, Xfl, Wq, Wk, Wv,
                                                       Qfh, Qfl, Kfh, Kfl, QfT, KfT, VfT);
     sfreq_kernel<<<dim3(NF, BATCHN), 256, 0, stream>>>(Qfh, Qfl, Kfh, Kfl, Sre, Sim);
-    rmean_kernel<<<dim3(SEQ / 64, BATCHN), 256, 0, stream>>>(Sre, Sim, Rm);
-    topk_kernel<<<BATCHN, 64, 0, stream>>>(Rm, Ti, Tw);
-    inv128_f<<<dim3(8, 16, 6), 256, 0, stream>>>(Gt, QfT, KfT, VfT, Qt, Kt, VT);
-    attn_kernel<<<dim3(SEQ / 128, NHEADS, BATCHN), 256, 0, stream>>>(Qt, Kt, VT, TO);
-    combine_kernel<<<dim3(HID / 256, SEQ, BATCHN), 256, 0, stream>>>(TO, Vm, Ti, Tw, Yc);
-    gemm128_nt<<<dim3(8, 32), 256, 0, stream>>>(flag, Yc, Wo, bo, d_out, 1);
-}
+    mega5_kernel<<<832, 256, 0, stream>>>(Gt, QfT, KfT, VfT, Qt, Kt, VT, Sre, Sim, Rm);
+    mega6_kernel<<<514, 256, 0, stream>>>(Qt, Kt, VT, TO, Rm, Ti, Tw);
+    combine_kernel<<<dim3(SEQ / 2, BATCHN), 256, 0, stream>>>(TO, Vm, Ti, Tw, Yc);
+    gemmO_kernel<<<dim3(8, 32), 256, 0, stream>>>(flag, Yc, Wo, bo, d_out);
+}
```

Measured after the change: 410.3 us. 5.4% less time.
